# Optimization experiments

Measured on AMD Instinct MI355X. Metric: run time of the kernel, lower is better.

## Reference

```python
import jax, jax.numpy as jnp
import numpy as np
import math

N_NODES = 100000
N_EDGES = 1600000
IN_FEATS = 128
H_FEATS = 64
NUM_CLASSES = 2
D = 2  # num_layers -> d+1 = 3 filters, each polynomial of degree d


def _calc_thetas(d):
    # Beta-Bernstein polynomial coefficients, ascending powers of x.
    # f_i(x) = (x/2)^i (1-x/2)^(d-i) / B(i+1, d+1-i),  B = i!(d-i)!/(d+1)!
    thetas = []
    for i in range(d + 1):
        beta = math.factorial(i) * math.factorial(d - i) / math.factorial(d + 1)
        p = np.array([1.0])
        for _ in range(i):
            p = np.convolve(p, [0.0, 0.5])
        for _ in range(d - i):
            p = np.convolve(p, [1.0, -0.5])
        thetas.append([float(c) for c in (p / beta)])
    return thetas

THETAS = _calc_thetas(D)


def setup_inputs() -> dict:
    key = jax.random.key(0)
    ks = jax.random.split(key, 12)
    x = jax.random.normal(ks[0], (N_NODES, IN_FEATS), dtype=jnp.float32)
    edge_index = jax.random.randint(ks[1], (2, N_EDGES), 0, N_NODES, dtype=jnp.int64)
    s = 0.05
    W1 = jax.random.normal(ks[2], (IN_FEATS, H_FEATS), jnp.float32) * s
    b1 = jnp.zeros((H_FEATS,), jnp.float32)
    W2 = jax.random.normal(ks[3], (H_FEATS, H_FEATS), jnp.float32) * s
    b2 = jnp.zeros((H_FEATS,), jnp.float32)
    Wm1 = jax.random.normal(ks[4], (H_FEATS * len(THETAS), H_FEATS), jnp.float32) * s
    bm1 = jnp.zeros((H_FEATS,), jnp.float32)
    Wm2 = jax.random.normal(ks[5], (H_FEATS, NUM_CLASSES), jnp.float32) * s
    bm2 = jnp.zeros((NUM_CLASSES,), jnp.float32)
    return {"x": x, "edge_index": edge_index, "W1": W1, "b1": b1,
            "W2": W2, "b2": b2, "Wm1": Wm1, "bm1": bm1, "Wm2": Wm2, "bm2": bm2}


def reference(x, edge_index, W1, b1, W2, b2, Wm1, bm1, Wm2, bm2):
    N = x.shape[0]
    src, dst = edge_index[0], edge_index[1]
    # in-degrees (edges point src -> dst, message summed at dst)
    deg = jax.ops.segment_sum(jnp.ones((edge_index.shape[1],), x.dtype), dst,
                              num_segments=N)
    dinv = jnp.clip(deg, 1.0, None) ** -0.5  # [N]
    dinv = dinv[:, None]
    # two linear + ReLU layers
    h = jax.nn.relu(x @ W1 + b1)
    h = jax.nn.relu(h @ W2 + b2)
    # PolyConv per theta: feat <- feat - D^-1/2 A D^-1/2 feat; acc += theta_k feat
    outs = []
    for theta in THETAS:
        feat = h
        acc = theta[0] * feat
        for k in range(1, len(theta)):
            msg = jax.ops.segment_sum((feat * dinv)[src], dst, num_segments=N)
            feat = feat - msg * dinv
            acc = acc + theta[k] * feat
        outs.append(acc)
    h_final = jnp.concatenate(outs, axis=-1)  # [N, h_feats*(d+1)]
    # MLP (2 layers): Linear -> ReLU -> Linear
    h_final = jax.nn.relu(h_final @ Wm1 + bm1)
    return h_final @ Wm2 + bm2
```

## Files before the change

kernel.cpp:

```cpp
#include <hip/hip_runtime.h>
#include <math.h>

#define N_NODES 100000
#define N_EDGES 1600000
#define IN_F 128
#define H_F 64
#define KP 68

#define NBKT 196
#define BSEG 16384
#define BCAP 14336

#define NP        100096
#define OFF_CNT   0
#define OFF_MPK   256
#define OFF_OFFS  (256 + 6144)
#define OFF_D2    (OFF_OFFS + NP + 64)
#define OFF_RD    (OFF_D2 + NP)
#define OFF_DINV  (OFF_RD + NP)
#define OFF_ADJ   (OFF_DINV + NP)
#define OFF_H0    (OFF_ADJ + N_EDGES)
#define OFF_H1    (OFF_H0 + N_NODES*32)
#define OFF_H2    (OFF_H1 + N_NODES*32)

typedef __attribute__((ext_vector_type(8))) short bf16x8;
typedef __attribute__((ext_vector_type(4))) float f32x4;

__device__ __forceinline__ unsigned short bf16rn(float f) {
    unsigned u = __float_as_uint(f);
    u += 0x7FFFu + ((u >> 16) & 1u);
    return (unsigned short)(u >> 16);
}
__device__ __forceinline__ float4 bf4tof(ushort4 h) {
    float4 f;
    f.x = __uint_as_float((unsigned)h.x << 16);
    f.y = __uint_as_float((unsigned)h.y << 16);
    f.z = __uint_as_float((unsigned)h.z << 16);
    f.w = __uint_as_float((unsigned)h.w << 16);
    return f;
}
#define UNPK(u, lo, hi) { lo = __uint_as_float((u) << 16); hi = __uint_as_float((u) & 0xFFFF0000u); }

__global__ __launch_bounds__(256) void k_bin(const int* __restrict__ src,
        const int* __restrict__ dst, int* __restrict__ cnt,
        int* __restrict__ binned, int E) {
    __shared__ int hist[NBKT];
    __shared__ int curb[NBKT];
    int t = threadIdx.x;
    for (int i = t; i < NBKT; i += 256) hist[i] = 0;
    __syncthreads();
    int base = blockIdx.x * 4096 + t;
    int d[16];
    #pragma unroll
    for (int i = 0; i < 16; ++i) {
        int e = base + i * 256;
        int dd = (e < E) ? dst[e] : -1;
        d[i] = dd;
        if (dd >= 0) atomicAdd(&hist[dd >> 9], 1);
    }
    __syncthreads();
    for (int i = t; i < NBKT; i += 256) {
        int h = hist[i];
        curb[i] = (h > 0) ? atomicAdd(&cnt[i], h) : 0;
    }
    __syncthreads();
    #pragma unroll
    for (int i = 0; i < 16; ++i) {
        int e = base + i * 256;
        if (e < E) {
            int s = src[e];
            int dd = d[i];
            int b = dd >> 9;
            int p = atomicAdd(&curb[b], 1);
            if (p < BSEG) binned[b * BSEG + p] = ((dd & 511) << 17) | s;
        }
    }
}

__global__ __launch_bounds__(256) void k_cfill(const int* __restrict__ binned,
        const int* __restrict__ cnt, int* __restrict__ offs, int* __restrict__ adj,
        float* __restrict__ d2a, float* __restrict__ rda, float* __restrict__ dinva) {
    __shared__ int csum[256];
    __shared__ int degl[512];
    __shared__ int offl[512];
    __shared__ int curl[512];
    __shared__ int wsum[4];
    __shared__ int adjl[BCAP];
    int b = blockIdx.x, t = threadIdx.x;
    int cv = (t < NBKT) ? cnt[t] : 0;
    csum[t] = cv;
    __syncthreads();
    #pragma unroll
    for (int off = 1; off < 256; off <<= 1) {
        int u = (t >= off) ? csum[t - off] : 0;
        __syncthreads();
        csum[t] += u;
        __syncthreads();
    }
    int baseb = (b == 0) ? 0 : csum[b - 1];
    int cntb = csum[b] - baseb;
    if (b == 0 && t == 0) offs[N_NODES] = N_EDGES;
    int n0 = b << 9;
    const int* bp = binned + b * BSEG;
    degl[2 * t] = 0; degl[2 * t + 1] = 0;
    __syncthreads();
    for (int i = t; i < cntb; i += 256) {
        int w = bp[i];
        atomicAdd(&degl[w >> 17], 1);
    }
    __syncthreads();
    int d0 = degl[2 * t], d1 = degl[2 * t + 1];
    int tot = d0 + d1;
    int lane = t & 63, wid = t >> 6;
    int inc = tot;
    #pragma unroll
    for (int off = 1; off < 64; off <<= 1) {
        int v = __shfl_up(inc, off, 64);
        if (lane >= off) inc += v;
    }
    if (lane == 63) wsum[wid] = inc;
    __syncthreads();
    int wb = 0;
    for (int w = 0; w < wid; ++w) wb += wsum[w];
    int excl = wb + inc - tot;
    offl[2 * t] = excl;          curl[2 * t] = excl;
    offl[2 * t + 1] = excl + d0; curl[2 * t + 1] = excl + d0;
    __syncthreads();
    #pragma unroll
    for (int rep = 0; rep < 2; ++rep) {
        int i = t + rep * 256;
        int n = n0 + i;
        if (n < N_NODES) {
            offs[n] = baseb + offl[i];
            float df = (float)degl[i];
            if (df < 1.f) df = 1.f;
            float di = 1.0f / sqrtf(df);
            dinva[n] = di;
            d2a[n] = di * di;
            rda[n] = sqrtf(df);
        }
    }
    for (int i = t; i < cntb; i += 256) {
        int w = bp[i];
        int loc = w >> 17;
        int s = w & 0x1FFFF;
        int p = atomicAdd(&curl[loc], 1);
        if (p < BCAP) adjl[p] = s;
        else adj[baseb + p] = s;
    }
    __syncthreads();
    int lim = cntb < BCAP ? cntb : BCAP;
    for (int i = t; i < lim; i += 256) adj[baseb + i] = adjl[i];
}

__global__ __launch_bounds__(256) void k_mcat(const float* __restrict__ Wm1,
                                              unsigned short* __restrict__ mpk) {
    int idx = blockIdx.x * 256 + threadIdx.x;
    if (idx >= 12288) return;
    int j = idx & 7;
    int n = (idx >> 3) & 63;
    int qd = (idx >> 9) & 3;
    int s = idx >> 11;
    int k = s * 32 + qd * 8 + j;
    int p = k >> 6;
    int kk = k & 63;
    float w0 = Wm1[kk * 64 + n];
    float w1 = Wm1[(64 + kk) * 64 + n];
    float w2 = Wm1[(128 + kk) * 64 + n];
    float v;
    if (p == 0)      v = 3.0f * w0;
    else if (p == 1) v = 3.0f * (w1 - w0);
    else             v = 0.75f * (w0 + w2) - 1.5f * w1;
    mpk[idx] = bf16rn(v);
}

__global__ __launch_bounds__(256) void k_gemm12(const float* __restrict__ x,
        const float* __restrict__ W1, const float* __restrict__ b1,
        const float* __restrict__ W2, const float* __restrict__ b2,
        const float* __restrict__ dinva, unsigned short* __restrict__ gsh, int N) {
    __shared__ float Al[64 * KP];
    __shared__ float Bl[64 * 64];
    __shared__ float Hl[64 * KP];
    int t = threadIdx.x;
    int tx = t & 15, ty = t >> 4;
    int nb = blockIdx.x * 64;
    float acc[4][4] = {{0}};
    for (int p = 0; p < 2; ++p) {
        #pragma unroll
        for (int pp = 0; pp < 4; ++pp) {
            int nl = ty + 16 * pp;
            int nn = nb + nl; if (nn >= N) nn = N - 1;
            float4 v = ((const float4*)(x + (size_t)nn * IN_F + p * 64))[tx];
            *(float4*)&Al[nl * KP + 4 * tx] = v;
        }
        #pragma unroll
        for (int pp = 0; pp < 4; ++pp) {
            int k = ty + 16 * pp;
            float4 v = ((const float4*)(W1 + (size_t)(p * 64 + k) * 64))[tx];
            *(float4*)&Bl[k * 64 + 4 * tx] = v;
        }
        __syncthreads();
        #pragma unroll 4
        for (int k = 0; k < 64; ++k) {
            float a0 = Al[(4 * ty + 0) * KP + k];
            float a1 = Al[(4 * ty + 1) * KP + k];
            float a2 = Al[(4 * ty + 2) * KP + k];
            float a3 = Al[(4 * ty + 3) * KP + k];
            float4 bv = *(const float4*)&Bl[k * 64 + 4 * tx];
            acc[0][0] = fmaf(a0, bv.x, acc[0][0]); acc[0][1] = fmaf(a0, bv.y, acc[0][1]);
            acc[0][2] = fmaf(a0, bv.z, acc[0][2]); acc[0][3] = fmaf(a0, bv.w, acc[0][3]);
            acc[1][0] = fmaf(a1, bv.x, acc[1][0]); acc[1][1] = fmaf(a1, bv.y, acc[1][1]);
            acc[1][2] = fmaf(a1, bv.z, acc[1][2]); acc[1][3] = fmaf(a1, bv.w, acc[1][3]);
            acc[2][0] = fmaf(a2, bv.x, acc[2][0]); acc[2][1] = fmaf(a2, bv.y, acc[2][1]);
            acc[2][2] = fmaf(a2, bv.z, acc[2][2]); acc[2][3] = fmaf(a2, bv.w, acc[2][3]);
            acc[3][0] = fmaf(a3, bv.x, acc[3][0]); acc[3][1] = fmaf(a3, bv.y, acc[3][1]);
            acc[3][2] = fmaf(a3, bv.z, acc[3][2]); acc[3][3] = fmaf(a3, bv.w, acc[3][3]);
        }
        __syncthreads();
    }
    {
        float4 bias = ((const float4*)b1)[tx];
        #pragma unroll
        for (int i = 0; i < 4; ++i) {
            float4 r;
            r.x = fmaxf(acc[i][0] + bias.x, 0.f);
            r.y = fmaxf(acc[i][1] + bias.y, 0.f);
            r.z = fmaxf(acc[i][2] + bias.z, 0.f);
            r.w = fmaxf(acc[i][3] + bias.w, 0.f);
            *(float4*)&Hl[(4 * ty + i) * KP + 4 * tx] = r;
            acc[i][0] = 0.f; acc[i][1] = 0.f; acc[i][2] = 0.f; acc[i][3] = 0.f;
        }
        #pragma unroll
        for (int pp = 0; pp < 4; ++pp) {
            int k = ty + 16 * pp;
            float4 v = ((const float4*)(W2 + (size_t)k * 64))[tx];
            *(float4*)&Bl[k * 64 + 4 * tx] = v;
        }
    }
    __syncthreads();
    #pragma unroll 4
    for (int k = 0; k < 64; ++k) {
        float a0 = Hl[(4 * ty + 0) * KP + k];
        float a1 = Hl[(4 * ty + 1) * KP + k];
        float a2 = Hl[(4 * ty + 2) * KP + k];
        float a3 = Hl[(4 * ty + 3) * KP + k];
        float4 bv = *(const float4*)&Bl[k * 64 + 4 * tx];
        acc[0][0] = fmaf(a0, bv.x, acc[0][0]); acc[0][1] = fmaf(a0, bv.y, acc[0][1]);
        acc[0][2] = fmaf(a0, bv.z, acc[0][2]); acc[0][3] = fmaf(a0, bv.w, acc[0][3]);
        acc[1][0] = fmaf(a1, bv.x, acc[1][0]); acc[1][1] = fmaf(a1, bv.y, acc[1][1]);
        acc[1][2] = fmaf(a1, bv.z, acc[1][2]); acc[1][3] = fmaf(a1, bv.w, acc[1][3]);
        acc[2][0] = fmaf(a2, bv.x, acc[2][0]); acc[2][1] = fmaf(a2, bv.y, acc[2][1]);
        acc[2][2] = fmaf(a2, bv.z, acc[2][2]); acc[2][3] = fmaf(a2, bv.w, acc[2][3]);
        acc[3][0] = fmaf(a3, bv.x, acc[3][0]); acc[3][1] = fmaf(a3, bv.y, acc[3][1]);
        acc[3][2] = fmaf(a3, bv.z, acc[3][2]); acc[3][3] = fmaf(a3, bv.w, acc[3][3]);
    }
    float4 bias2 = ((const float4*)b2)[tx];
    #pragma unroll
    for (int i = 0; i < 4; ++i) {
        int n = nb + 4 * ty + i;
        if (n < N) {
            float di = dinva[n];
            ushort4 hh;
            hh.x = bf16rn(di * fmaxf(acc[i][0] + bias2.x, 0.f));
            hh.y = bf16rn(di * fmaxf(acc[i][1] + bias2.y, 0.f));
            hh.z = bf16rn(di * fmaxf(acc[i][2] + bias2.z, 0.f));
            hh.w = bf16rn(di * fmaxf(acc[i][3] + bias2.w, 0.f));
            *(ushort4*)(gsh + (size_t)n * 64 + 4 * tx) = hh;
        }
    }
}

__global__ __launch_bounds__(256) void k_prop(const unsigned short* __restrict__ gh,
        unsigned short* __restrict__ gout, const int* __restrict__ offs,
        const int* __restrict__ adj, const float* __restrict__ d2a, int N) {
    int t = threadIdx.x;
    int lane = t & 63;
    int g = lane >> 3;
    int q = lane & 7;
    int n = blockIdx.x * 4 + (t >> 6);
    if (n >= N) return;
    int beg = offs[n], end = offs[n + 1];
    float a0 = 0.f, a1 = 0.f, a2 = 0.f, a3 = 0.f;
    float a4 = 0.f, a5 = 0.f, a6 = 0.f, a7 = 0.f;
    int e = beg + g;
    for (; e + 24 < end; e += 32) {
        int s0 = adj[e], s1 = adj[e + 8], s2 = adj[e + 16], s3 = adj[e + 24];
        uint4 v0 = *(const uint4*)(gh + (size_t)s0 * 64 + 8 * q);
        uint4 v1 = *(const uint4*)(gh + (size_t)s1 * 64 + 8 * q);
        uint4 v2 = *(const uint4*)(gh + (size_t)s2 * 64 + 8 * q);
        uint4 v3 = *(const uint4*)(gh + (size_t)s3 * 64 + 8 * q);
        float l, h;
        UNPK(v0.x, l, h); a0 += l; a1 += h;
        UNPK(v0.y, l, h); a2 += l; a3 += h;
        UNPK(v0.z, l, h); a4 += l; a5 += h;
        UNPK(v0.w, l, h); a6 += l; a7 += h;
        UNPK(v1.x, l, h); a0 += l; a1 += h;
        UNPK(v1.y, l, h); a2 += l; a3 += h;
        UNPK(v1.z, l, h); a4 += l; a5 += h;
        UNPK(v1.w, l, h); a6 += l; a7 += h;
        UNPK(v2.x, l, h); a0 += l; a1 += h;
        UNPK(v2.y, l, h); a2 += l; a3 += h;
        UNPK(v2.z, l, h); a4 += l; a5 += h;
        UNPK(v2.w, l, h); a6 += l; a7 += h;
        UNPK(v3.x, l, h); a0 += l; a1 += h;
        UNPK(v3.y, l, h); a2 += l; a3 += h;
        UNPK(v3.z, l, h); a4 += l; a5 += h;
        UNPK(v3.w, l, h); a6 += l; a7 += h;
    }
    for (; e < end; e += 8) {
        int s = adj[e];
        uint4 v = *(const uint4*)(gh + (size_t)s * 64 + 8 * q);
        float l, h;
        UNPK(v.x, l, h); a0 += l; a1 += h;
        UNPK(v.y, l, h); a2 += l; a3 += h;
        UNPK(v.z, l, h); a4 += l; a5 += h;
        UNPK(v.w, l, h); a6 += l; a7 += h;
    }
    #pragma unroll
    for (int m = 8; m < 64; m <<= 1) {
        a0 += __shfl_xor(a0, m); a1 += __shfl_xor(a1, m);
        a2 += __shfl_xor(a2, m); a3 += __shfl_xor(a3, m);
        a4 += __shfl_xor(a4, m); a5 += __shfl_xor(a5, m);
        a6 += __shfl_xor(a6, m); a7 += __shfl_xor(a7, m);
    }
    if (g == 0) {
        float d2n = d2a[n];
        uint4 sv = *(const uint4*)(gh + (size_t)n * 64 + 8 * q);
        float l, h;
        uint4 r;
        UNPK(sv.x, l, h);
        r.x = ((unsigned)bf16rn(fmaf(-d2n, a1, h)) << 16) | bf16rn(fmaf(-d2n, a0, l));
        UNPK(sv.y, l, h);
        r.y = ((unsigned)bf16rn(fmaf(-d2n, a3, h)) << 16) | bf16rn(fmaf(-d2n, a2, l));
        UNPK(sv.z, l, h);
        r.z = ((unsigned)bf16rn(fmaf(-d2n, a5, h)) << 16) | bf16rn(fmaf(-d2n, a4, l));
        UNPK(sv.w, l, h);
        r.w = ((unsigned)bf16rn(fmaf(-d2n, a7, h)) << 16) | bf16rn(fmaf(-d2n, a6, l));
        *(uint4*)(gout + (size_t)n * 64 + 8 * q) = r;
    }
}

__global__ __launch_bounds__(256) void k_final(const unsigned short* __restrict__ g0h,
        const unsigned short* __restrict__ g1h, const unsigned short* __restrict__ g2h,
        const unsigned short* __restrict__ mpk, const float* __restrict__ bm1,
        const float* __restrict__ Wm2, const float* __restrict__ bm2,
        const float* __restrict__ rda, float* __restrict__ out, int N) {
    int t = threadIdx.x;
    int w = t >> 6, lane = t & 63;
    int c = lane & 15, qd = lane >> 4;
    int nbase = blockIdx.x * 64 + w * 16;
    if (nbase >= N) return;
    int node = nbase + c;
    int nclamp = (node < N) ? node : N - 1;
    const unsigned short* bufs[3] = {g0h, g1h, g2h};
    f32x4 acc0 = {0.f, 0.f, 0.f, 0.f};
    f32x4 acc1 = {0.f, 0.f, 0.f, 0.f};
    f32x4 acc2 = {0.f, 0.f, 0.f, 0.f};
    f32x4 acc3 = {0.f, 0.f, 0.f, 0.f};
    #pragma unroll
    for (int s = 0; s < 6; ++s) {
        const unsigned short* gp = bufs[s >> 1];
        int k0 = (s & 1) * 32;
        bf16x8 a = *(const bf16x8*)(gp + (size_t)nclamp * 64 + k0 + qd * 8);
        const unsigned short* mb = mpk + (size_t)((s * 4 + qd) * 64) * 8;
        bf16x8 b0 = *(const bf16x8*)(mb + (size_t)(c) * 8);
        bf16x8 b1 = *(const bf16x8*)(mb + (size_t)(16 + c) * 8);
        bf16x8 b2 = *(const bf16x8*)(mb + (size_t)(32 + c) * 8);
        bf16x8 b3 = *(const bf16x8*)(mb + (size_t)(48 + c) * 8);
        acc0 = __builtin_amdgcn_mfma_f32_16x16x32_bf16(a, b0, acc0, 0, 0, 0);
        acc1 = __builtin_amdgcn_mfma_f32_16x16x32_bf16(a, b1, acc1, 0, 0, 0);
        acc2 = __builtin_amdgcn_mfma_f32_16x16x32_bf16(a, b2, acc2, 0, 0, 0);
        acc3 = __builtin_amdgcn_mfma_f32_16x16x32_bf16(a, b3, acc3, 0, 0, 0);
    }
    float rdr[4];
    #pragma unroll
    for (int r = 0; r < 4; ++r) {
        int nd = nbase + qd * 4 + r;
        rdr[r] = rda[(nd < N) ? nd : N - 1];
    }
    float p0[4] = {0.f, 0.f, 0.f, 0.f};
    float p1[4] = {0.f, 0.f, 0.f, 0.f};
    #pragma unroll
    for (int ot = 0; ot < 4; ++ot) {
        int col = ot * 16 + c;
        float bmc = bm1[col];
        float wc0 = Wm2[col * 2 + 0];
        float wc1 = Wm2[col * 2 + 1];
        f32x4 a = (ot == 0) ? acc0 : (ot == 1) ? acc1 : (ot == 2) ? acc2 : acc3;
        #pragma unroll
        for (int r = 0; r < 4; ++r) {
            float h = fmaxf(fmaf(rdr[r], a[r], bmc), 0.f);
            p0[r] = fmaf(h, wc0, p0[r]);
            p1[r] = fmaf(h, wc1, p1[r]);
        }
    }
    #pragma unroll
    for (int m = 1; m < 16; m <<= 1) {
        #pragma unroll
        for (int r = 0; r < 4; ++r) {
            p0[r] += __shfl_xor(p0[r], m);
            p1[r] += __shfl_xor(p1[r], m);
        }
    }
    if (c == 0) {
        float bo0 = bm2[0], bo1 = bm2[1];
        #pragma unroll
        for (int r = 0; r < 4; ++r) {
            int nd = nbase + qd * 4 + r;
            if (nd < N) {
                float2 o;
                o.x = p0[r] + bo0;
                o.y = p1[r] + bo1;
                *(float2*)(out + (size_t)nd * 2) = o;
            }
        }
    }
}

extern "C" void kernel_launch(void* const* d_in, const int* in_sizes, int n_in,
                              void* d_out, int out_size, void* d_ws, size_t ws_size,
                              hipStream_t stream) {
    const float* x   = (const float*)d_in[0];
    const int*   ei  = (const int*)d_in[1];
    const float* W1  = (const float*)d_in[2];
    const float* b1  = (const float*)d_in[3];
    const float* W2  = (const float*)d_in[4];
    const float* b2  = (const float*)d_in[5];
    const float* Wm1 = (const float*)d_in[6];
    const float* bm1 = (const float*)d_in[7];
    const float* Wm2 = (const float*)d_in[8];
    const float* bm2 = (const float*)d_in[9];
    float* out = (float*)d_out;

    int* ws = (int*)d_ws;
    int*   cnt   = ws + OFF_CNT;
    unsigned short* mpk = (unsigned short*)(ws + OFF_MPK);
    int*   offs  = ws + OFF_OFFS;
    float* d2a   = (float*)(ws + OFF_D2);
    float* rda   = (float*)(ws + OFF_RD);
    float* dinva = (float*)(ws + OFF_DINV);
    int*   adj   = ws + OFF_ADJ;
    unsigned short* gs0h = (unsigned short*)(ws + OFF_H0);
    unsigned short* gs1h = (unsigned short*)(ws + OFF_H1);
    unsigned short* gs2h = (unsigned short*)(ws + OFF_H2);
    int*   binned = ws + OFF_H1;

    const int* srcp = ei;
    const int* dstp = ei + N_EDGES;

    hipMemsetAsync(cnt, 0, 256 * sizeof(int), stream);

    k_mcat<<<48, 256, 0, stream>>>(Wm1, mpk);
    k_bin<<<(N_EDGES + 4095) / 4096, 256, 0, stream>>>(srcp, dstp, cnt, binned, N_EDGES);
    k_cfill<<<NBKT, 256, 0, stream>>>(binned, cnt, offs, adj, d2a, rda, dinva);

    int nblk = (N_NODES + 63) / 64;
    k_gemm12<<<nblk, 256, 0, stream>>>(x, W1, b1, W2, b2, dinva, gs0h, N_NODES);

    k_prop<<<(N_NODES + 3) / 4, 256, 0, stream>>>(gs0h, gs1h, offs, adj, d2a, N_NODES);
    k_prop<<<(N_NODES + 3) / 4, 256, 0, stream>>>(gs1h, gs2h, offs, adj, d2a, N_NODES);

    k_final<<<nblk, 256, 0, stream>>>(gs0h, gs1h, gs2h, mpk, bm1, Wm2, bm2, rda, out, N_NODES);
}
```

Before: 285.4 us.

## Use split-bf16 MFMA for input MLP GEMMs and per-wave histograms in binning

Replaces the fp32 FMA tiled GEMM for the two input linear layers with bf16 MFMA 16x16x32, using a hi/lo split (three products per step) to keep close to fp32 accuracy. Weights are pre-split and laid out in MFMA order by a merged prep kernel, and each wave handles 16 nodes with no block-wide syncs. Separately, the edge-binning kernel keeps per-wave shared histograms to reduce LDS atomic contention. The cost is three times the MFMA work plus conversion overhead, and a small rounding difference from the fp32 path.

```diff
diff --git a/kernel.cpp b/kernel.cpp
--- a/kernel.cpp
+++ b/kernel.cpp
@@ -5,7 +5,6 @@
 #define N_EDGES 1600000
 #define IN_F 128
 #define H_F 64
-#define KP 68
 
 #define NBKT 196
 #define BSEG 16384
@@ -14,7 +13,11 @@
 #define NP        100096
 #define OFF_CNT   0
 #define OFF_MPK   256
-#define OFF_OFFS  (256 + 6144)
+#define OFF_W1H   6400
+#define OFF_W1L   10496
+#define OFF_W2H   14592
+#define OFF_W2L   16640
+#define OFF_OFFS  18688
 #define OFF_D2    (OFF_OFFS + NP + 64)
 #define OFF_RD    (OFF_D2 + NP)
 #define OFF_DINV  (OFF_RD + NP)
@@ -31,23 +34,57 @@
     u += 0x7FFFu + ((u >> 16) & 1u);
     return (unsigned short)(u >> 16);
 }
-__device__ __forceinline__ float4 bf4tof(ushort4 h) {
-    float4 f;
-    f.x = __uint_as_float((unsigned)h.x << 16);
-    f.y = __uint_as_float((unsigned)h.y << 16);
-    f.z = __uint_as_float((unsigned)h.z << 16);
-    f.w = __uint_as_float((unsigned)h.w << 16);
-    return f;
-}
 #define UNPK(u, lo, hi) { lo = __uint_as_float((u) << 16); hi = __uint_as_float((u) & 0xFFFF0000u); }
+
+__global__ __launch_bounds__(256) void k_prep(const float* __restrict__ Wm1,
+        const float* __restrict__ W1, const float* __restrict__ W2,
+        unsigned short* __restrict__ mpk,
+        unsigned short* __restrict__ w1h, unsigned short* __restrict__ w1l,
+        unsigned short* __restrict__ w2h, unsigned short* __restrict__ w2l) {
+    int idx = blockIdx.x * 256 + threadIdx.x;
+    if (idx < 12288) {
+        int j = idx & 7;
+        int n = (idx >> 3) & 63;
+        int qd = (idx >> 9) & 3;
+        int s = idx >> 11;
+        int k = s * 32 + qd * 8 + j;
+        int p = k >> 6;
+        int kk = k & 63;
+        float w0 = Wm1[kk * 64 + n];
+        float w1 = Wm1[(64 + kk) * 64 + n];
+        float w2 = Wm1[(128 + kk) * 64 + n];
+        float v;
+        if (p == 0)      v = 3.0f * w0;
+        else if (p == 1) v = 3.0f * (w1 - w0);
+        else             v = 0.75f * (w0 + w2) - 1.5f * w1;
+        mpk[idx] = bf16rn(v);
+    } else if (idx < 12288 + 8192) {
+        int lin = idx - 12288;
+        int j = lin & 7, cc = (lin >> 3) & 15, ot = (lin >> 7) & 3;
+        int qd = (lin >> 9) & 3, ks = lin >> 11;
+        float v = W1[(ks * 32 + qd * 8 + j) * 64 + ot * 16 + cc];
+        unsigned short h = bf16rn(v);
+        w1h[lin] = h;
+        w1l[lin] = bf16rn(v - __uint_as_float((unsigned)h << 16));
+    } else if (idx < 24576) {
+        int lin = idx - 20480;
+        int j = lin & 7, cc = (lin >> 3) & 15, ot = (lin >> 7) & 3;
+        int qd = (lin >> 9) & 3, ks = lin >> 11;
+        float v = W2[(ks * 32 + qd * 8 + j) * 64 + ot * 16 + cc];
+        unsigned short h = bf16rn(v);
+        w2h[lin] = h;
+        w2l[lin] = bf16rn(v - __uint_as_float((unsigned)h << 16));
+    }
+}
 
 __global__ __launch_bounds__(256) void k_bin(const int* __restrict__ src,
         const int* __restrict__ dst, int* __restrict__ cnt,
         int* __restrict__ binned, int E) {
-    __shared__ int hist[NBKT];
-    __shared__ int curb[NBKT];
+    __shared__ int hist[4][208];
+    __shared__ int cur4[4][208];
     int t = threadIdx.x;
-    for (int i = t; i < NBKT; i += 256) hist[i] = 0;
+    int w = t >> 6;
+    for (int i = t; i < 4 * 208; i += 256) (&hist[0][0])[i] = 0;
     __syncthreads();
     int base = blockIdx.x * 4096 + t;
     int d[16];
@@ -56,12 +93,17 @@
         int e = base + i * 256;
         int dd = (e < E) ? dst[e] : -1;
         d[i] = dd;
-        if (dd >= 0) atomicAdd(&hist[dd >> 9], 1);
-    }
-    __syncthreads();
-    for (int i = t; i < NBKT; i += 256) {
-        int h = hist[i];
-        curb[i] = (h > 0) ? atomicAdd(&cnt[i], h) : 0;
+        if (dd >= 0) atomicAdd(&hist[w][dd >> 9], 1);
+    }
+    __syncthreads();
+    if (t < NBKT) {
+        int h0 = hist[0][t], h1 = hist[1][t], h2 = hist[2][t], h3 = hist[3][t];
+        int tot = h0 + h1 + h2 + h3;
+        int b0 = (tot > 0) ? atomicAdd(&cnt[t], tot) : 0;
+        cur4[0][t] = b0;
+        cur4[1][t] = b0 + h0;
+        cur4[2][t] = b0 + h0 + h1;
+        cur4[3][t] = b0 + h0 + h1 + h2;
     }
     __syncthreads();
     #pragma unroll
@@ -71,7 +113,7 @@
             int s = src[e];
             int dd = d[i];
             int b = dd >> 9;
-            int p = atomicAdd(&curb[b], 1);
+            int p = atomicAdd(&cur4[w][b], 1);
             if (p < BSEG) binned[b * BSEG + p] = ((dd & 511) << 17) | s;
         }
     }
@@ -153,119 +195,125 @@
     for (int i = t; i < lim; i += 256) adj[baseb + i] = adjl[i];
 }
 
-__global__ __launch_bounds__(256) void k_mcat(const float* __restrict__ Wm1,
-                                              unsigned short* __restrict__ mpk) {
-    int idx = blockIdx.x * 256 + threadIdx.x;
-    if (idx >= 12288) return;
-    int j = idx & 7;
-    int n = (idx >> 3) & 63;
-    int qd = (idx >> 9) & 3;
-    int s = idx >> 11;
-    int k = s * 32 + qd * 8 + j;
-    int p = k >> 6;
-    int kk = k & 63;
-    float w0 = Wm1[kk * 64 + n];
-    float w1 = Wm1[(64 + kk) * 64 + n];
-    float w2 = Wm1[(128 + kk) * 64 + n];
-    float v;
-    if (p == 0)      v = 3.0f * w0;
-    else if (p == 1) v = 3.0f * (w1 - w0);
-    else             v = 0.75f * (w0 + w2) - 1.5f * w1;
-    mpk[idx] = bf16rn(v);
-}
-
 __global__ __launch_bounds__(256) void k_gemm12(const float* __restrict__ x,
-        const float* __restrict__ W1, const float* __restrict__ b1,
-        const float* __restrict__ W2, const float* __restrict__ b2,
+        const unsigned short* __restrict__ w1h, const unsigned short* __restrict__ w1l,
+        const unsigned short* __restrict__ w2h, const unsigned short* __restrict__ w2l,
+        const float* __restrict__ b1, const float* __restrict__ b2,
         const float* __restrict__ dinva, unsigned short* __restrict__ gsh, int N) {
-    __shared__ float Al[64 * KP];
-    __shared__ float Bl[64 * 64];
-    __shared__ float Hl[64 * KP];
+    __shared__ unsigned int Hl[4][16 * 65];
+    __shared__ unsigned short Sl[4][16 * 66];
     int t = threadIdx.x;
-    int tx = t & 15, ty = t >> 4;
-    int nb = blockIdx.x * 64;
-    float acc[4][4] = {{0}};
-    for (int p = 0; p < 2; ++p) {
-        #pragma unroll
-        for (int pp = 0; pp < 4; ++pp) {
-            int nl = ty + 16 * pp;
-            int nn = nb + nl; if (nn >= N) nn = N - 1;
-            float4 v = ((const float4*)(x + (size_t)nn * IN_F + p * 64))[tx];
-            *(float4*)&Al[nl * KP + 4 * tx] = v;
-        }
-        #pragma unroll
-        for (int pp = 0; pp < 4; ++pp) {
-            int k = ty + 16 * pp;
-            float4 v = ((const float4*)(W1 + (size_t)(p * 64 + k) * 64))[tx];
-            *(float4*)&Bl[k * 64 + 4 * tx] = v;
-        }
-        __syncthreads();
-        #pragma unroll 4
-        for (int k = 0; k < 64; ++k) {
-            float a0 = Al[(4 * ty + 0) * KP + k];
-            float a1 = Al[(4 * ty + 1) * KP + k];
-            float a2 = Al[(4 * ty + 2) * KP + k];
-            float a3 = Al[(4 * ty + 3) * KP + k];
-            float4 bv = *(const float4*)&Bl[k * 64 + 4 * tx];
-            acc[0][0] = fmaf(a0, bv.x, acc[0][0]); acc[0][1] = fmaf(a0, bv.y, acc[0][1]);
-            acc[0][2] = fmaf(a0, bv.z, acc[0][2]); acc[0][3] = fmaf(a0, bv.w, acc[0][3]);
-            acc[1][0] = fmaf(a1, bv.x, acc[1][0]); acc[1][1] = fmaf(a1, bv.y, acc[1][1]);
-            acc[1][2] = fmaf(a1, bv.z, acc[1][2]); acc[1][3] = fmaf(a1, bv.w, acc[1][3]);
-            acc[2][0] = fmaf(a2, bv.x, acc[2][0]); acc[2][1] = fmaf(a2, bv.y, acc[2][1]);
-            acc[2][2] = fmaf(a2, bv.z, acc[2][2]); acc[2][3] = fmaf(a2, bv.w, acc[2][3]);
-            acc[3][0] = fmaf(a3, bv.x, acc[3][0]); acc[3][1] = fmaf(a3, bv.y, acc[3][1]);
-            acc[3][2] = fmaf(a3, bv.z, acc[3][2]); acc[3][3] = fmaf(a3, bv.w, acc[3][3]);
-        }
-        __syncthreads();
-    }
-    {
-        float4 bias = ((const float4*)b1)[tx];
-        #pragma unroll
-        for (int i = 0; i < 4; ++i) {
-            float4 r;
-            r.x = fmaxf(acc[i][0] + bias.x, 0.f);
-            r.y = fmaxf(acc[i][1] + bias.y, 0.f);
-            r.z = fmaxf(acc[i][2] + bias.z, 0.f);
-            r.w = fmaxf(acc[i][3] + bias.w, 0.f);
-            *(float4*)&Hl[(4 * ty + i) * KP + 4 * tx] = r;
-            acc[i][0] = 0.f; acc[i][1] = 0.f; acc[i][2] = 0.f; acc[i][3] = 0.f;
-        }
-        #pragma unroll
-        for (int pp = 0; pp < 4; ++pp) {
-            int k = ty + 16 * pp;
-            float4 v = ((const float4*)(W2 + (size_t)k * 64))[tx];
-            *(float4*)&Bl[k * 64 + 4 * tx] = v;
-        }
-    }
-    __syncthreads();
-    #pragma unroll 4
-    for (int k = 0; k < 64; ++k) {
-        float a0 = Hl[(4 * ty + 0) * KP + k];
-        float a1 = Hl[(4 * ty + 1) * KP + k];
-        float a2 = Hl[(4 * ty + 2) * KP + k];
-        float a3 = Hl[(4 * ty + 3) * KP + k];
-        float4 bv = *(const float4*)&Bl[k * 64 + 4 * tx];
-        acc[0][0] = fmaf(a0, bv.x, acc[0][0]); acc[0][1] = fmaf(a0, bv.y, acc[0][1]);
-        acc[0][2] = fmaf(a0, bv.z, acc[0][2]); acc[0][3] = fmaf(a0, bv.w, acc[0][3]);
-        acc[1][0] = fmaf(a1, bv.x, acc[1][0]); acc[1][1] = fmaf(a1, bv.y, acc[1][1]);
-        acc[1][2] = fmaf(a1, bv.z, acc[1][2]); acc[1][3] = fmaf(a1, bv.w, acc[1][3]);
-        acc[2][0] = fmaf(a2, bv.x, acc[2][0]); acc[2][1] = fmaf(a2, bv.y, acc[2][1]);
-        acc[2][2] = fmaf(a2, bv.z, acc[2][2]); acc[2][3] = fmaf(a2, bv.w, acc[2][3]);
-        acc[3][0] = fmaf(a3, bv.x, acc[3][0]); acc[3][1] = fmaf(a3, bv.y, acc[3][1]);
-        acc[3][2] = fmaf(a3, bv.z, acc[3][2]); acc[3][3] = fmaf(a3, bv.w, acc[3][3]);
-    }
-    float4 bias2 = ((const float4*)b2)[tx];
+    int w = t >> 6, lane = t & 63;
+    int c = lane & 15, qd = lane >> 4;
+    int nbase = blockIdx.x * 64 + w * 16;
+    if (nbase >= N) return;
+    int node = nbase + c;
+    int nclamp = (node < N) ? node : N - 1;
+
+    f32x4 a0 = {0.f,0.f,0.f,0.f}, a1 = a0, a2 = a0, a3 = a0;
+    #pragma unroll
+    for (int ks = 0; ks < 4; ++ks) {
+        const float* xp = x + (size_t)nclamp * IN_F + ks * 32 + qd * 8;
+        float4 xa = *(const float4*)xp;
+        float4 xb = *(const float4*)(xp + 4);
+        float xs[8] = {xa.x, xa.y, xa.z, xa.w, xb.x, xb.y, xb.z, xb.w};
+        bf16x8 ahi, alo;
+        #pragma unroll
+        for (int j = 0; j < 8; ++j) {
+            unsigned short h = bf16rn(xs[j]);
+            ahi[j] = (short)h;
+            alo[j] = (short)bf16rn(xs[j] - __uint_as_float((unsigned)h << 16));
+        }
+        const unsigned short* bh = w1h + (size_t)(ks * 4 + qd) * 512;
+        const unsigned short* bl = w1l + (size_t)(ks * 4 + qd) * 512;
+        bf16x8 h0 = *(const bf16x8*)(bh + 0 * 128 + c * 8);
+        bf16x8 l0 = *(const bf16x8*)(bl + 0 * 128 + c * 8);
+        bf16x8 h1 = *(const bf16x8*)(bh + 1 * 128 + c * 8);
+        bf16x8 l1 = *(const bf16x8*)(bl + 1 * 128 + c * 8);
+        bf16x8 h2 = *(const bf16x8*)(bh + 2 * 128 + c * 8);
+        bf16x8 l2 = *(const bf16x8*)(bl + 2 * 128 + c * 8);
+        bf16x8 h3 = *(const bf16x8*)(bh + 3 * 128 + c * 8);
+        bf16x8 l3 = *(const bf16x8*)(bl + 3 * 128 + c * 8);
+        a0 = __builtin_amdgcn_mfma_f32_16x16x32_bf16(ahi, h0, a0, 0, 0, 0);
+        a1 = __builtin_amdgcn_mfma_f32_16x16x32_bf16(ahi, h1, a1, 0, 0, 0);
+        a2 = __builtin_amdgcn_mfma_f32_16x16x32_bf16(ahi, h2, a2, 0, 0, 0);
+        a3 = __builtin_amdgcn_mfma_f32_16x16x32_bf16(ahi, h3, a3, 0, 0, 0);
+        a0 = __builtin_amdgcn_mfma_f32_16x16x32_bf16(alo, h0, a0, 0, 0, 0);
+        a1 = __builtin_amdgcn_mfma_f32_16x16x32_bf16(alo, h1, a1, 0, 0, 0);
+        a2 = __builtin_amdgcn_mfma_f32_16x16x32_bf16(alo, h2, a2, 0, 0, 0);
+        a3 = __builtin_amdgcn_mfma_f32_16x16x32_bf16(alo, h3, a3, 0, 0, 0);
+        a0 = __builtin_amdgcn_mfma_f32_16x16x32_bf16(ahi, l0, a0, 0, 0, 0);
+        a1 = __builtin_amdgcn_mfma_f32_16x16x32_bf16(ahi, l1, a1, 0, 0, 0);
+        a2 = __builtin_amdgcn_mfma_f32_16x16x32_bf16(ahi, l2, a2, 0, 0, 0);
+        a3 = __builtin_amdgcn_mfma_f32_16x16x32_bf16(ahi, l3, a3, 0, 0, 0);
+    }
+    #pragma unroll
+    for (int ot = 0; ot < 4; ++ot) {
+        float bb = b1[ot * 16 + c];
+        f32x4 a = (ot == 0) ? a0 : (ot == 1) ? a1 : (ot == 2) ? a2 : a3;
+        #pragma unroll
+        for (int r = 0; r < 4; ++r) {
+            float h = fmaxf(a[r] + bb, 0.f);
+            unsigned short hh = bf16rn(h);
+            unsigned short hl = bf16rn(h - __uint_as_float((unsigned)hh << 16));
+            Hl[w][(qd * 4 + r) * 65 + ot * 16 + c] = ((unsigned)hh << 16) | hl;
+        }
+    }
+    f32x4 d0 = {0.f,0.f,0.f,0.f}, d1 = d0, d2 = d0, d3 = d0;
+    #pragma unroll
+    for (int ks = 0; ks < 2; ++ks) {
+        bf16x8 ahi, alo;
+        #pragma unroll
+        for (int j = 0; j < 8; ++j) {
+            unsigned v = Hl[w][c * 65 + ks * 32 + qd * 8 + j];
+            ahi[j] = (short)(v >> 16);
+            alo[j] = (short)(v & 0xFFFFu);
+        }
+        const unsigned short* bh = w2h + (size_t)(ks * 4 + qd) * 512;
+        const unsigned short* bl = w2l + (size_t)(ks * 4 + qd) * 512;
+        bf16x8 h0 = *(const bf16x8*)(bh + 0 * 128 + c * 8);
+        bf16x8 l0 = *(const bf16x8*)(bl + 0 * 128 + c * 8);
+        bf16x8 h1 = *(const bf16x8*)(bh + 1 * 128 + c * 8);
+        bf16x8 l1 = *(const bf16x8*)(bl + 1 * 128 + c * 8);
+        bf16x8 h2 = *(const bf16x8*)(bh + 2 * 128 + c * 8);
+        bf16x8 l2 = *(const bf16x8*)(bl + 2 * 128 + c * 8);
+        bf16x8 h3 = *(const bf16x8*)(bh + 3 * 128 + c * 8);
+        bf16x8 l3 = *(const bf16x8*)(bl + 3 * 128 + c * 8);
+        d0 = __builtin_amdgcn_mfma_f32_16x16x32_bf16(ahi, h0, d0, 0, 0, 0);
+        d1 = __builtin_amdgcn_mfma_f32_16x16x32_bf16(ahi, h1, d1, 0, 0, 0);
+        d2 = __builtin_amdgcn_mfma_f32_16x16x32_bf16(ahi, h2, d2, 0, 0, 0);
+        d3 = __builtin_amdgcn_mfma_f32_16x16x32_bf16(ahi, h3, d3, 0, 0, 0);
+        d0 = __builtin_amdgcn_mfma_f32_16x16x32_bf16(alo, h0, d0, 0, 0, 0);
+        d1 = __builtin_amdgcn_mfma_f32_16x16x32_bf16(alo, h1, d1, 0, 0, 0);
+        d2 = __builtin_amdgcn_mfma_f32_16x16x32_bf16(alo, h2, d2, 0, 0, 0);
+        d3 = __builtin_amdgcn_mfma_f32_16x16x32_bf16(alo, h3, d3, 0, 0, 0);
+        d0 = __builtin_amdgcn_mfma_f32_16x16x32_bf16(ahi, l0, d0, 0, 0, 0);
+        d1 = __builtin_amdgcn_mfma_f32_16x16x32_bf16(ahi, l1, d1, 0, 0, 0);
+        d2 = __builtin_amdgcn_mfma_f32_16x16x32_bf16(ahi, l2, d2, 0, 0, 0);
+        d3 = __builtin_amdgcn_mfma_f32_16x16x32_bf16(ahi, l3, d3, 0, 0, 0);
+    }
+    #pragma unroll
+    for (int ot = 0; ot < 4; ++ot) {
+        float bb = b2[ot * 16 + c];
+        f32x4 a = (ot == 0) ? d0 : (ot == 1) ? d1 : (ot == 2) ? d2 : d3;
+        #pragma unroll
+        for (int r = 0; r < 4; ++r) {
+            int nd = nbase + qd * 4 + r;
+            float di = dinva[(nd < N) ? nd : N - 1];
+            Sl[w][(qd * 4 + r) * 66 + ot * 16 + c] = bf16rn(di * fmaxf(a[r] + bb, 0.f));
+        }
+    }
     #pragma unroll
     for (int i = 0; i < 4; ++i) {
-        int n = nb + 4 * ty + i;
-        if (n < N) {
-            float di = dinva[n];
-            ushort4 hh;
-            hh.x = bf16rn(di * fmaxf(acc[i][0] + bias2.x, 0.f));
-            hh.y = bf16rn(di * fmaxf(acc[i][1] + bias2.y, 0.f));
-            hh.z = bf16rn(di * fmaxf(acc[i][2] + bias2.z, 0.f));
-            hh.w = bf16rn(di * fmaxf(acc[i][3] + bias2.w, 0.f));
-            *(ushort4*)(gsh + (size_t)n * 64 + 4 * tx) = hh;
+        int nl = i * 4 + qd;
+        int nd = nbase + nl;
+        if (nd < N) {
+            ushort4 v;
+            v.x = Sl[w][nl * 66 + c * 4 + 0];
+            v.y = Sl[w][nl * 66 + c * 4 + 1];
+            v.z = Sl[w][nl * 66 + c * 4 + 2];
+            v.w = Sl[w][nl * 66 + c * 4 + 3];
+            *(ushort4*)(gsh + (size_t)nd * 64 + c * 4) = v;
         }
     }
 }
@@ -435,6 +483,10 @@
     int* ws = (int*)d_ws;
     int*   cnt   = ws + OFF_CNT;
     unsigned short* mpk = (unsigned short*)(ws + OFF_MPK);
+    unsigned short* w1h = (unsigned short*)(ws + OFF_W1H);
+    unsigned short* w1l = (unsigned short*)(ws + OFF_W1L);
+    unsigned short* w2h = (unsigned short*)(ws + OFF_W2H);
+    unsigned short* w2l = (unsigned short*)(ws + OFF_W2L);
     int*   offs  = ws + OFF_OFFS;
     float* d2a   = (float*)(ws + OFF_D2);
     float* rda   = (float*)(ws + OFF_RD);
@@ -450,12 +502,12 @@
 
     hipMemsetAsync(cnt, 0, 256 * sizeof(int), stream);
 
-    k_mcat<<<48, 256, 0, stream>>>(Wm1, mpk);
+    k_prep<<<96, 256, 0, stream>>>(Wm1, W1, W2, mpk, w1h, w1l, w2h, w2l);
     k_bin<<<(N_EDGES + 4095) / 4096, 256, 0, stream>>>(srcp, dstp, cnt, binned, N_EDGES);
     k_cfill<<<NBKT, 256, 0, stream>>>(binned, cnt, offs, adj, d2a, rda, dinva);
 
     int nblk = (N_NODES + 63) / 64;
-    k_gemm12<<<nblk, 256, 0, stream>>>(x, W1, b1, W2, b2, dinva, gs0h, N_NODES);
+    k_gemm12<<<nblk, 256, 0, stream>>>(x, w1h, w1l, w2h, w2l, b1, b2, dinva, gs0h, N_NODES);
 
     k_prop<<<(N_NODES + 3) / 4, 256, 0, stream>>>(gs0h, gs1h, offs, adj, d2a, N_NODES);
     k_prop<<<(N_NODES + 3) / 4, 256, 0, stream>>>(gs1h, gs2h, offs, adj, d2a, N_NODES);
```

Result: faster. 270.1 us (-5.4%).
